# Kernel optimization log

Hardware: AMD Instinct MI355X
Metric: run time of the kernel (lower is better)

The kernel has to match this reference:

```python
import jax, jax.numpy as jnp
import numpy as np

N = 100000
E = 3200000
F_IN = 512
HID = 16
N_CLS = 40


def setup_inputs() -> dict:
    key = jax.random.key(0)
    k1, k2, k3, k4, k5, k6 = jax.random.split(key, 6)
    x = jax.random.normal(k1, (N, F_IN), dtype=jnp.float32)
    edge_index = jax.random.randint(k2, (2, E), 0, N, dtype=jnp.int64)
    # Glorot-ish init for layer weights (as in PyG GCNConv defaults)
    W1 = jax.random.normal(k3, (F_IN, HID), dtype=jnp.float32) * (1.0 / np.sqrt(F_IN))
    b1 = jnp.zeros((HID,), dtype=jnp.float32)
    W2 = jax.random.normal(k4, (HID, N_CLS), dtype=jnp.float32) * (1.0 / np.sqrt(HID))
    b2 = jnp.zeros((N_CLS,), dtype=jnp.float32)
    return {"x": x, "W1": W1, "b1": b1, "W2": W2, "b2": b2, "edge_index": edge_index}


def _gcn_norm(edge_index, n):
    # Add self-loops, compute symmetric normalization deg^{-1/2} (A+I) deg^{-1/2}
    loops = jnp.arange(n, dtype=edge_index.dtype)
    src = jnp.concatenate([edge_index[0], loops])  # [E+N]
    dst = jnp.concatenate([edge_index[1], loops])  # [E+N]
    ones = jnp.ones(src.shape, dtype=jnp.float32)
    deg = jax.ops.segment_sum(ones, dst, num_segments=n)  # in-degree with self-loops
    dinv = jnp.where(deg > 0, jax.lax.rsqrt(deg), 0.0)
    norm = dinv[src] * dinv[dst]  # [E+N]
    return src, dst, norm


def _gcn_conv(h, W, b, src, dst, norm, n):
    h = h @ W  # transform first (cheaper: small out dim)
    msg = h[src] * norm[:, None]           # gather + scale
    out = jax.ops.segment_sum(msg, dst, num_segments=n)  # scatter-add
    return out + b


def reference(x, W1, b1, W2, b2, edge_index):
    n = x.shape[0]
    src, dst, norm = _gcn_norm(edge_index, n)
    h = _gcn_conv(x, W1, b1, src, dst, norm, n)
    h = jax.nn.relu(h)
    # F.dropout(training=self.training): identity in eval mode
    h = _gcn_conv(h, W2, b2, src, dst, norm, n)
    return jax.nn.log_softmax(h, axis=1)
```

## Files before the change

### kernel.cpp

```cpp
#include <hip/hip_runtime.h>

typedef __attribute__((ext_vector_type(8))) short short8;
typedef __attribute__((ext_vector_type(4))) float floatx4;

#define CHUNK 8192
#define SHIFT 8
#define BCAP 12288

__device__ __forceinline__ short f2bf(float f) {
    unsigned int u = __float_as_uint(f);
    u = (u + 0x7FFFu + ((u >> 16) & 1u)) >> 16;
    return (short)u;
}


__global__ void scan_part(const int* __restrict__ cnt, int* __restrict__ bsums, int N) {
    __shared__ int sh[256];
    int tid = threadIdx.x;
    int base = blockIdx.x * 1024 + tid * 4;
    int s = 0;
#pragma unroll
    for (int j = 0; j < 4; ++j) { int idx = base + j; if (idx < N) s += cnt[idx]; }
    sh[tid] = s; __syncthreads();
    for (int d = 128; d > 0; d >>= 1) { if (tid < d) sh[tid] += sh[tid + d]; __syncthreads(); }
    if (tid == 0) bsums[blockIdx.x] = sh[0];
}

__global__ void scan_small(int* __restrict__ b, int nb) {
    __shared__ int s[1024];
    int tid = threadIdx.x;
    int v = (tid < nb) ? b[tid] : 0;
    s[tid] = v; __syncthreads();
    for (int d = 1; d < 1024; d <<= 1) {
        int t = (tid >= d) ? s[tid - d] : 0;
        __syncthreads();
        s[tid] += t;
        __syncthreads();
    }
    if (tid < nb) b[tid] = s[tid] - v;
}

__global__ __launch_bounds__(256) void scan_apply(int* __restrict__ v, const int* __restrict__ bsums, int M) {
    __shared__ int sh[256];
    int tid = threadIdx.x;
    int base = blockIdx.x * 1024 + tid * 4;
    int x[4]; int tsum = 0;
#pragma unroll
    for (int j = 0; j < 4; ++j) { int idx = base + j; x[j] = (idx < M) ? v[idx] : 0; tsum += x[j]; }
    sh[tid] = tsum; __syncthreads();
    for (int d = 1; d < 256; d <<= 1) {
        int t = (tid >= d) ? sh[tid - d] : 0;
        __syncthreads();
        sh[tid] += t;
        __syncthreads();
    }
    int run = sh[tid] - tsum + bsums[blockIdx.x];
#pragma unroll
    for (int j = 0; j < 4; ++j) {
        int idx = base + j;
        if (idx < M) { v[idx] = run; run += x[j]; }
    }
}


__global__ __launch_bounds__(256) void blockhist(const int* __restrict__ dst, int* __restrict__ ghist,
                                                 int E, int nbuk, int nblk) {
    __shared__ int lh[512];
    int tid = threadIdx.x, blk = blockIdx.x;
    for (int i = tid; i < nbuk; i += 256) lh[i] = 0;
    __syncthreads();
    int base = blk * CHUNK;
    int end = base + CHUNK; if (end > E) end = E;
    for (int i = base + tid; i < end; i += 256)
        atomicAdd(&lh[dst[i] >> SHIFT], 1);
    __syncthreads();
    for (int i = tid; i < nbuk; i += 256) ghist[(size_t)i * nblk + blk] = lh[i];
}

__global__ __launch_bounds__(256) void binpass(const int* __restrict__ eidx, const int* __restrict__ ghist,
                                               unsigned* __restrict__ ebin, int E, int nbuk, int nblk) {
    __shared__ int lh[512];
    __shared__ int lb[512];
    int tid = threadIdx.x, blk = blockIdx.x;
    for (int i = tid; i < nbuk; i += 256) { lh[i] = 0; lb[i] = ghist[(size_t)i * nblk + blk]; }
    __syncthreads();
    int base = blk * CHUNK;
    int end = base + CHUNK; if (end > E) end = E;
    for (int i = base + tid; i < end; i += 256) {
        unsigned s = (unsigned)eidx[i];
        unsigned d = (unsigned)eidx[E + i];
        int buk = d >> SHIFT;
        int r = atomicAdd(&lh[buk], 1);
        ebin[lb[buk] + r] = s | ((d & 255u) << 24);
    }
}

__global__ __launch_bounds__(256) void permB(const int* __restrict__ ghist, int nblk, int nbuk,
                                             int* __restrict__ off, int* __restrict__ cnt,
                                             float* __restrict__ dinv,
                                             const unsigned* __restrict__ ebin,
                                             unsigned* __restrict__ efin,
                                             int N, int E) {
    __shared__ unsigned stage[BCAP];
    __shared__ int hist[256];
    __shared__ int sc[256];
    __shared__ int obase[256];
    __shared__ int lcur[256];
    int k = blockIdx.x, tid = threadIdx.x;
    int n0 = k << SHIFT;
    int bstart = ghist[(size_t)k * nblk];
    int bend = (k + 1 < nbuk) ? ghist[(size_t)(k + 1) * nblk] : E;
    int cntb = bend - bstart;
    hist[tid] = 0;
    __syncthreads();
    for (int i = tid; i < cntb; i += 256) {
        unsigned p = ebin[bstart + i];
        if (i < BCAP) stage[i] = p;
        atomicAdd(&hist[p >> 24], 1);
    }
    __syncthreads();
    int h = hist[tid];
    sc[tid] = h; __syncthreads();
    for (int d = 1; d < 256; d <<= 1) {
        int t = (tid >= d) ? sc[tid - d] : 0;
        __syncthreads();
        sc[tid] += t;
        __syncthreads();
    }
    int excl = sc[tid] - h;
    int nn = n0 + tid;
    if (nn < N) {
        off[nn] = bstart + excl;
        cnt[nn] = h;
        dinv[nn] = rsqrtf((float)(h + 1));
    }
    obase[tid] = bstart + excl;
    lcur[tid] = 0;
    __syncthreads();
    for (int i = tid; i < cntb; i += 256) {
        unsigned p = (i < BCAP) ? stage[i] : ebin[bstart + i];
        int d = p >> 24;
        int r = atomicAdd(&lcur[d], 1);
        efin[obase[d] + r] = p & 0xFFFFFFu;
    }
}

__global__ __launch_bounds__(256) void gemm1_mfma(const float* __restrict__ x,
                                                  const float* __restrict__ w1,
                                                  const float* __restrict__ dinv,
                                                  float* __restrict__ g1,
                                                  int ntiles, int N) {
    __shared__ __align__(16) float wl[512 * 16];
    int tid = threadIdx.x;
    for (int i = tid; i < 2048; i += 256)
        ((float4*)wl)[i] = ((const float4*)w1)[i];
    __syncthreads();

    int lane = tid & 63;
    int q = lane >> 4, r = lane & 15;

    short8 bf[16];
#pragma unroll
    for (int kk = 0; kk < 16; ++kk) {
        int kb = kk * 32 + q * 8;
        short8 t;
#pragma unroll
        for (int j = 0; j < 8; ++j) t[j] = f2bf(wl[(kb + j) * 16 + r]);
        bf[kk] = t;
    }

    int tile = blockIdx.x * 4 + (tid >> 6);
    if (tile >= ntiles) return;
    int nb = tile * 16;
    int row = nb + r; if (row >= N) row = N - 1;
    const float* xp = x + (size_t)row * 512 + q * 8;
    floatx4 acc = {0.f, 0.f, 0.f, 0.f};
#pragma unroll
    for (int kk = 0; kk < 16; ++kk) {
        float4 a0 = *(const float4*)(xp + kk * 32);
        float4 a1 = *(const float4*)(xp + kk * 32 + 4);
        short8 af;
        af[0] = f2bf(a0.x); af[1] = f2bf(a0.y); af[2] = f2bf(a0.z); af[3] = f2bf(a0.w);
        af[4] = f2bf(a1.x); af[5] = f2bf(a1.y); af[6] = f2bf(a1.z); af[7] = f2bf(a1.w);
        acc = __builtin_amdgcn_mfma_f32_16x16x32_bf16(af, bf[kk], acc, 0, 0, 0);
    }
#pragma unroll
    for (int i = 0; i < 4; ++i) {
        int rr = nb + q * 4 + i;
        if (rr < N) g1[(size_t)rr * 16 + r] = acc[i] * dinv[rr];
    }
}

__global__ __launch_bounds__(256) void agg16w(const float* __restrict__ in, float* __restrict__ out,
                                              const int* __restrict__ off, const int* __restrict__ cnt,
                                              const float* __restrict__ dinv,
                                              const unsigned* __restrict__ edges,
                                              const float* __restrict__ bias, int N) {
    int t = blockIdx.x * blockDim.x + threadIdx.x;
    int n = t >> 6;
    if (n >= N) return;
    int lane = t & 63;
    int h = lane & 15, j = lane >> 4;
    int p0 = off[n], c = cnt[n];
    const unsigned* ep = edges + p0;
    float acc = 0.0f;
    for (int i = j; i < c; i += 4) {
        unsigned s = ep[i];
        acc += in[s * 16 + h];
    }
    acc += __shfl_xor(acc, 16, 64);
    acc += __shfl_xor(acc, 32, 64);
    if (j == 0) {
        float di = dinv[n];
        float v = di * (acc + in[n * 16 + h]);
        if (bias) v = fmaxf(v + bias[h], 0.0f) * di;
        out[n * 16 + h] = v;
    }
}

__global__ __launch_bounds__(256) void out_ls(const float* __restrict__ a2,
                                              const float* __restrict__ w2,
                                              const float* __restrict__ b2,
                                              float* __restrict__ out, int N) {
    __shared__ float w2s[704];
    __shared__ float b2s[40];
    int tid = threadIdx.x;
    for (int i = tid; i < 704; i += 256) w2s[i] = (i < 640) ? w2[i] : 0.0f;
    if (tid < 40) b2s[tid] = b2[tid];
    __syncthreads();
    int lane = tid & 63;
    int n = blockIdx.x * 4 + (tid >> 6);
    if (n >= N) return;
    const float* ar = a2 + (size_t)n * 16;
    bool act = lane < 40;
    float acc = act ? b2s[lane] : 0.0f;
#pragma unroll
    for (int k = 0; k < 16; ++k) {
        float av = ar[k];
        acc += av * w2s[k * 40 + lane];
    }
    float v = act ? acc : -__builtin_inff();
#pragma unroll
    for (int s = 32; s > 0; s >>= 1) v = fmaxf(v, __shfl_xor(v, s, 64));
    float ex = act ? expf(acc - v) : 0.0f;
    float ssum = ex;
#pragma unroll
    for (int s = 32; s > 0; s >>= 1) ssum += __shfl_xor(ssum, s, 64);
    float lse = logf(ssum);
    if (act) out[(size_t)n * 40 + lane] = acc - v - lse;
}


extern "C" void kernel_launch(void* const* d_in, const int* in_sizes, int n_in,
                              void* d_out, int out_size, void* d_ws, size_t ws_size,
                              hipStream_t stream) {
    const float* x   = (const float*)d_in[0];
    const float* W1  = (const float*)d_in[1];
    const float* b1  = (const float*)d_in[2];
    const float* W2  = (const float*)d_in[3];
    const float* b2  = (const float*)d_in[4];
    const int*   eidx = (const int*)d_in[5];
    float* out = (float*)d_out;

    const int N = in_sizes[0] / 512;
    const int E = in_sizes[5] / 2;

    const int NBUK = (N + 255) >> SHIFT;
    const int nblk = (E + CHUNK - 1) / CHUNK;
    const int M = NBUK * nblk;

    char* w = (char*)d_ws;
    auto alloc = [&](size_t bytes) { char* p = w; w += (bytes + 255) & ~(size_t)255; return p; };
    int*      off   = (int*)alloc((size_t)N * 4);
    int*      cnt   = (int*)alloc((size_t)N * 4);
    float*    dinv  = (float*)alloc((size_t)N * 4);
    int*      bsums = (int*)alloc(1024 * 4);
    int*      ghist = (int*)alloc((size_t)M * 4);
    unsigned* ebin  = (unsigned*)alloc((size_t)E * 4);
    unsigned* efin  = (unsigned*)alloc((size_t)E * 4);
    float* g1 = (float*)ebin;
    float* r1 = g1 + (size_t)N * 16;
    float* a2 = g1;

    int mb = (M + 1023) / 1024;

    blockhist<<<nblk, 256, 0, stream>>>(eidx + E, ghist, E, NBUK, nblk);
    scan_part<<<mb, 256, 0, stream>>>(ghist, bsums, M);
    scan_small<<<1, 1024, 0, stream>>>(bsums, mb);
    scan_apply<<<mb, 256, 0, stream>>>(ghist, bsums, M);
    binpass<<<nblk, 256, 0, stream>>>(eidx, ghist, ebin, E, NBUK, nblk);
    permB<<<NBUK, 256, 0, stream>>>(ghist, nblk, NBUK, off, cnt, dinv, ebin, efin, N, E);

    int ntiles = (N + 15) / 16;
    gemm1_mfma<<<(ntiles + 3) / 4, 256, 0, stream>>>(x, W1, dinv, g1, ntiles, N);

    agg16w<<<((size_t)N * 64 + 255) / 256, 256, 0, stream>>>(g1, r1, off, cnt, dinv, (const unsigned*)efin, b1, N);
    agg16w<<<((size_t)N * 64 + 255) / 256, 256, 0, stream>>>(r1, a2, off, cnt, dinv, (const unsigned*)efin, (const float*)nullptr, N);

    out_ls<<<(N + 3) / 4, 256, 0, stream>>>(a2, W2, b2, out, N);
}
```

Baseline: 615.6 us.

## Vectorize neighbor gathers to float4 and fuse second aggregation with output layer

The aggregation kernel now has each lane load a float4 slice of a neighbor's 16-wide feature row, so 16 edges are processed per wave iteration instead of 4, and the partial sums are combined with a longer shuffle reduction. The second aggregation is merged with the W2 projection and log-softmax kernel, so the intermediate a2 buffer is never written to or read back from global memory and one launch is removed. In exchange, the reduction uses more shuffles, and agg16w now always reads the bias pointer because the null-bias path is gone.

```diff
diff --git a/kernel.cpp b/kernel.cpp
--- a/kernel.cpp
+++ b/kernel.cpp
@@ -191,6 +191,18 @@
     }
 }
 
+__device__ __forceinline__ float4 shfl_xor4(float4 v, int d) {
+    float4 r;
+    r.x = __shfl_xor(v.x, d, 64);
+    r.y = __shfl_xor(v.y, d, 64);
+    r.z = __shfl_xor(v.z, d, 64);
+    r.w = __shfl_xor(v.w, d, 64);
+    return r;
+}
+__device__ __forceinline__ float4 add4(float4 a, float4 b) {
+    return make_float4(a.x + b.x, a.y + b.y, a.z + b.z, a.w + b.w);
+}
+
 __global__ __launch_bounds__(256) void agg16w(const float* __restrict__ in, float* __restrict__ out,
                                               const int* __restrict__ off, const int* __restrict__ cnt,
                                               const float* __restrict__ dinv,
@@ -200,54 +212,86 @@
     int n = t >> 6;
     if (n >= N) return;
     int lane = t & 63;
-    int h = lane & 15, j = lane >> 4;
+    int h4 = lane & 3, j = lane >> 2;
     int p0 = off[n], c = cnt[n];
     const unsigned* ep = edges + p0;
-    float acc = 0.0f;
-    for (int i = j; i < c; i += 4) {
+    float4 acc = make_float4(0.f, 0.f, 0.f, 0.f);
+    for (int i = j; i < c; i += 16) {
         unsigned s = ep[i];
-        acc += in[s * 16 + h];
-    }
-    acc += __shfl_xor(acc, 16, 64);
-    acc += __shfl_xor(acc, 32, 64);
+        acc = add4(acc, *(const float4*)(in + (size_t)s * 16 + h4 * 4));
+    }
+#pragma unroll
+    for (int d = 4; d < 64; d <<= 1) acc = add4(acc, shfl_xor4(acc, d));
     if (j == 0) {
         float di = dinv[n];
-        float v = di * (acc + in[n * 16 + h]);
-        if (bias) v = fmaxf(v + bias[h], 0.0f) * di;
-        out[n * 16 + h] = v;
-    }
-}
-
-__global__ __launch_bounds__(256) void out_ls(const float* __restrict__ a2,
-                                              const float* __restrict__ w2,
-                                              const float* __restrict__ b2,
-                                              float* __restrict__ out, int N) {
+        float4 sv = *(const float4*)(in + (size_t)n * 16 + h4 * 4);
+        float4 b4 = *(const float4*)(bias + h4 * 4);
+        float4 v;
+        v.x = fmaxf(di * (acc.x + sv.x) + b4.x, 0.f) * di;
+        v.y = fmaxf(di * (acc.y + sv.y) + b4.y, 0.f) * di;
+        v.z = fmaxf(di * (acc.z + sv.z) + b4.z, 0.f) * di;
+        v.w = fmaxf(di * (acc.w + sv.w) + b4.w, 0.f) * di;
+        *(float4*)(out + (size_t)n * 16 + h4 * 4) = v;
+    }
+}
+
+__global__ __launch_bounds__(256) void agg_out(const float* __restrict__ in,
+                                               const int* __restrict__ off, const int* __restrict__ cnt,
+                                               const float* __restrict__ dinv,
+                                               const unsigned* __restrict__ edges,
+                                               const float* __restrict__ w2,
+                                               const float* __restrict__ b2,
+                                               float* __restrict__ out, int N) {
     __shared__ float w2s[704];
     __shared__ float b2s[40];
     int tid = threadIdx.x;
     for (int i = tid; i < 704; i += 256) w2s[i] = (i < 640) ? w2[i] : 0.0f;
     if (tid < 40) b2s[tid] = b2[tid];
     __syncthreads();
-    int lane = tid & 63;
+
     int n = blockIdx.x * 4 + (tid >> 6);
     if (n >= N) return;
-    const float* ar = a2 + (size_t)n * 16;
+    int lane = tid & 63;
+    int h4 = lane & 3, j = lane >> 2;
+    int p0 = off[n], c = cnt[n];
+    const unsigned* ep = edges + p0;
+    float4 acc = make_float4(0.f, 0.f, 0.f, 0.f);
+    for (int i = j; i < c; i += 16) {
+        unsigned s = ep[i];
+        acc = add4(acc, *(const float4*)(in + (size_t)s * 16 + h4 * 4));
+    }
+#pragma unroll
+    for (int d = 4; d < 64; d <<= 1) acc = add4(acc, shfl_xor4(acc, d));
+    float di = dinv[n];
+    float4 sv = *(const float4*)(in + (size_t)n * 16 + h4 * 4);
+    float4 v4;
+    v4.x = di * (acc.x + sv.x);
+    v4.y = di * (acc.y + sv.y);
+    v4.z = di * (acc.z + sv.z);
+    v4.w = di * (acc.w + sv.w);
+
+    float a2k[16];
+#pragma unroll
+    for (int k = 0; k < 16; ++k) {
+        float comp = (k & 3) == 0 ? v4.x : (k & 3) == 1 ? v4.y : (k & 3) == 2 ? v4.z : v4.w;
+        a2k[k] = __shfl(comp, k >> 2, 64);
+    }
+
     bool act = lane < 40;
-    float acc = act ? b2s[lane] : 0.0f;
-#pragma unroll
-    for (int k = 0; k < 16; ++k) {
-        float av = ar[k];
-        acc += av * w2s[k * 40 + lane];
-    }
-    float v = act ? acc : -__builtin_inff();
+    float dot = act ? b2s[lane] : 0.0f;
+#pragma unroll
+    for (int k = 0; k < 16; ++k)
+        dot += a2k[k] * w2s[k * 40 + lane];
+
+    float v = act ? dot : -__builtin_inff();
 #pragma unroll
     for (int s = 32; s > 0; s >>= 1) v = fmaxf(v, __shfl_xor(v, s, 64));
-    float ex = act ? expf(acc - v) : 0.0f;
+    float ex = act ? expf(dot - v) : 0.0f;
     float ssum = ex;
 #pragma unroll
     for (int s = 32; s > 0; s >>= 1) ssum += __shfl_xor(ssum, s, 64);
     float lse = logf(ssum);
-    if (act) out[(size_t)n * 40 + lane] = acc - v - lse;
+    if (act) out[(size_t)n * 40 + lane] = dot - v - lse;
 }
 
 
@@ -280,7 +324,6 @@
     unsigned* efin  = (unsigned*)alloc((size_t)E * 4);
     float* g1 = (float*)ebin;
     float* r1 = g1 + (size_t)N * 16;
-    float* a2 = g1;
 
     int mb = (M + 1023) / 1024;
 
@@ -295,7 +338,5 @@
     gemm1_mfma<<<(ntiles + 3) / 4, 256, 0, stream>>>(x, W1, dinv, g1, ntiles, N);
 
     agg16w<<<((size_t)N * 64 + 255) / 256, 256, 0, stream>>>(g1, r1, off, cnt, dinv, (const unsigned*)efin, b1, N);
-    agg16w<<<((size_t)N * 64 + 255) / 256, 256, 0, stream>>>(r1, a2, off, cnt, dinv, (const unsigned*)efin, (const float*)nullptr, N);
-
-    out_ls<<<(N + 3) / 4, 256, 0, stream>>>(a2, W2, b2, out, N);
-}
+    agg_out<<<(N + 3) / 4, 256, 0, stream>>>(r1, off, cnt, dinv, (const unsigned*)efin, W2, b2, out, N);
+}
```

Result: faster. 532.4 us (-13.5%).

## Split hidden features into two 8-wide halves and aggregate each with float4 gathers

Applied to the files above, without the earlier changes.

The GEMM writes the 16-wide hidden features as two separate 8-wide arrays, and each graph aggregation now runs as two passes, one per half. Each pass gathers float4 values, with 32 edges in flight per wavefront instead of 4, and reads edge indices with nontemporal loads. The goal is to halve the randomly gathered working set per pass so it caches better, and to raise memory-level parallelism. In exchange the edge list is read twice as often, there are extra kernel launches, and dedicated buffers are allocated instead of reusing the edge bin buffer.

```diff
diff --git a/kernel.cpp b/kernel.cpp
--- a/kernel.cpp
+++ b/kernel.cpp
@@ -148,7 +148,8 @@
 __global__ __launch_bounds__(256) void gemm1_mfma(const float* __restrict__ x,
                                                   const float* __restrict__ w1,
                                                   const float* __restrict__ dinv,
-                                                  float* __restrict__ g1,
+                                                  float* __restrict__ gA,
+                                                  float* __restrict__ gB,
                                                   int ntiles, int N) {
     __shared__ __align__(16) float wl[512 * 16];
     int tid = threadIdx.x;
@@ -184,41 +185,68 @@
         af[4] = f2bf(a1.x); af[5] = f2bf(a1.y); af[6] = f2bf(a1.z); af[7] = f2bf(a1.w);
         acc = __builtin_amdgcn_mfma_f32_16x16x32_bf16(af, bf[kk], acc, 0, 0, 0);
     }
+    float* base = (r < 8) ? gA : gB;
+    int col = r & 7;
 #pragma unroll
     for (int i = 0; i < 4; ++i) {
         int rr = nb + q * 4 + i;
-        if (rr < N) g1[(size_t)rr * 16 + r] = acc[i] * dinv[rr];
-    }
-}
-
-__global__ __launch_bounds__(256) void agg16w(const float* __restrict__ in, float* __restrict__ out,
-                                              const int* __restrict__ off, const int* __restrict__ cnt,
-                                              const float* __restrict__ dinv,
-                                              const unsigned* __restrict__ edges,
-                                              const float* __restrict__ bias, int N) {
+        if (rr < N) base[(size_t)rr * 8 + col] = acc[i] * dinv[rr];
+    }
+}
+
+__device__ __forceinline__ float4 shfl_xor4(float4 v, int d) {
+    float4 r;
+    r.x = __shfl_xor(v.x, d, 64);
+    r.y = __shfl_xor(v.y, d, 64);
+    r.z = __shfl_xor(v.z, d, 64);
+    r.w = __shfl_xor(v.w, d, 64);
+    return r;
+}
+__device__ __forceinline__ float4 add4(float4 a, float4 b) {
+    return make_float4(a.x + b.x, a.y + b.y, a.z + b.z, a.w + b.w);
+}
+
+__global__ __launch_bounds__(256) void agg8w(const float* __restrict__ in, float* __restrict__ out,
+                                             const int* __restrict__ off, const int* __restrict__ cnt,
+                                             const float* __restrict__ dinv,
+                                             const unsigned* __restrict__ edges,
+                                             const float* __restrict__ bias, int N) {
     int t = blockIdx.x * blockDim.x + threadIdx.x;
     int n = t >> 6;
     if (n >= N) return;
     int lane = t & 63;
-    int h = lane & 15, j = lane >> 4;
+    int h4 = lane & 1, j = lane >> 1;
     int p0 = off[n], c = cnt[n];
     const unsigned* ep = edges + p0;
-    float acc = 0.0f;
-    for (int i = j; i < c; i += 4) {
-        unsigned s = ep[i];
-        acc += in[s * 16 + h];
-    }
-    acc += __shfl_xor(acc, 16, 64);
-    acc += __shfl_xor(acc, 32, 64);
+    float4 acc = make_float4(0.f, 0.f, 0.f, 0.f);
+    for (int i = j; i < c; i += 32) {
+        unsigned s = __builtin_nontemporal_load(&ep[i]);
+        acc = add4(acc, *(const float4*)(in + (size_t)s * 8 + h4 * 4));
+    }
+#pragma unroll
+    for (int d = 2; d < 64; d <<= 1) acc = add4(acc, shfl_xor4(acc, d));
     if (j == 0) {
         float di = dinv[n];
-        float v = di * (acc + in[n * 16 + h]);
-        if (bias) v = fmaxf(v + bias[h], 0.0f) * di;
-        out[n * 16 + h] = v;
-    }
-}
-
-__global__ __launch_bounds__(256) void out_ls(const float* __restrict__ a2,
+        float4 sv = *(const float4*)(in + (size_t)n * 8 + h4 * 4);
+        float4 v;
+        if (bias) {
+            float4 b4 = *(const float4*)(bias + h4 * 4);
+            v.x = fmaxf(di * (acc.x + sv.x) + b4.x, 0.f) * di;
+            v.y = fmaxf(di * (acc.y + sv.y) + b4.y, 0.f) * di;
+            v.z = fmaxf(di * (acc.z + sv.z) + b4.z, 0.f) * di;
+            v.w = fmaxf(di * (acc.w + sv.w) + b4.w, 0.f) * di;
+        } else {
+            v.x = di * (acc.x + sv.x);
+            v.y = di * (acc.y + sv.y);
+            v.z = di * (acc.z + sv.z);
+            v.w = di * (acc.w + sv.w);
+        }
+        *(float4*)(out + (size_t)n * 8 + h4 * 4) = v;
+    }
+}
+
+__global__ __launch_bounds__(256) void out_ls(const float* __restrict__ a2a,
+                                              const float* __restrict__ a2b,
                                               const float* __restrict__ w2,
                                               const float* __restrict__ b2,
                                               float* __restrict__ out, int N) {
@@ -231,13 +259,14 @@
     int lane = tid & 63;
     int n = blockIdx.x * 4 + (tid >> 6);
     if (n >= N) return;
-    const float* ar = a2 + (size_t)n * 16;
+    const float* ara = a2a + (size_t)n * 8;
+    const float* arb = a2b + (size_t)n * 8;
     bool act = lane < 40;
     float acc = act ? b2s[lane] : 0.0f;
 #pragma unroll
-    for (int k = 0; k < 16; ++k) {
-        float av = ar[k];
-        acc += av * w2s[k * 40 + lane];
+    for (int k = 0; k < 8; ++k) {
+        acc += ara[k] * w2s[k * 40 + lane];
+        acc += arb[k] * w2s[(k + 8) * 40 + lane];
     }
     float v = act ? acc : -__builtin_inff();
 #pragma unroll
@@ -278,9 +307,12 @@
     int*      ghist = (int*)alloc((size_t)M * 4);
     unsigned* ebin  = (unsigned*)alloc((size_t)E * 4);
     unsigned* efin  = (unsigned*)alloc((size_t)E * 4);
-    float* g1 = (float*)ebin;
-    float* r1 = g1 + (size_t)N * 16;
-    float* a2 = g1;
+    float*    gA    = (float*)alloc((size_t)N * 8 * 4);
+    float*    gB    = (float*)alloc((size_t)N * 8 * 4);
+    float*    rA    = (float*)alloc((size_t)N * 8 * 4);
+    float*    rB    = (float*)alloc((size_t)N * 8 * 4);
+    float*    a2a   = gA;
+    float*    a2b   = gB;
 
     int mb = (M + 1023) / 1024;
 
@@ -292,10 +324,13 @@
     permB<<<NBUK, 256, 0, stream>>>(ghist, nblk, NBUK, off, cnt, dinv, ebin, efin, N, E);
 
     int ntiles = (N + 15) / 16;
-    gemm1_mfma<<<(ntiles + 3) / 4, 256, 0, stream>>>(x, W1, dinv, g1, ntiles, N);
-
-    agg16w<<<((size_t)N * 64 + 255) / 256, 256, 0, stream>>>(g1, r1, off, cnt, dinv, (const unsigned*)efin, b1, N);
-    agg16w<<<((size_t)N * 64 + 255) / 256, 256, 0, stream>>>(r1, a2, off, cnt, dinv, (const unsigned*)efin, (const float*)nullptr, N);
-
-    out_ls<<<(N + 3) / 4, 256, 0, stream>>>(a2, W2, b2, out, N);
-}
+    gemm1_mfma<<<(ntiles + 3) / 4, 256, 0, stream>>>(x, W1, dinv, gA, gB, ntiles, N);
+
+    size_t aggblocks = ((size_t)N * 64 + 255) / 256;
+    agg8w<<<aggblocks, 256, 0, stream>>>(gA, rA, off, cnt, dinv, (const unsigned*)efin, b1, N);
+    agg8w<<<aggblocks, 256, 0, stream>>>(gB, rB, off, cnt, dinv, (const unsigned*)efin, b1 + 8, N);
+    agg8w<<<aggblocks, 256, 0, stream>>>(rA, a2a, off, cnt, dinv, (const unsigned*)efin, (const float*)nullptr, N);
+    agg8w<<<aggblocks, 256, 0, stream>>>(rB, a2b, off, cnt, dinv, (const unsigned*)efin, (const float*)nullptr, N);
+
+    out_ls<<<(N + 3) / 4, 256, 0, stream>>>(a2a, a2b, W2, b2, out, N);
+}
```

Measured after the change: 622.1 us. About the same (+1.1%).
